# Performance work log

Measured on AMD Instinct MI355X. Metric: run time of the kernel, lower is better.

Reference implementation:

```python
import jax, jax.numpy as jnp
import numpy as np

BITS = 4
MAXQ = (1 << BITS) - 1  # 15
GROUPSIZE = 128
IN_F = 8192
OUT_F = 8192
PACK = 32 // BITS  # 8 values per int32


def setup_inputs() -> dict:
    key = jax.random.key(0)
    k_x, k_w, k_z, k_s, k_b = jax.random.split(key, 5)
    groups = IN_F // GROUPSIZE
    x = jax.random.normal(k_x, (4, 32, IN_F), dtype=jnp.float32)
    # bit-packed int32 weight / zeros (random bit patterns are valid quantized data)
    qweight = jax.random.randint(k_w, (IN_F // PACK, OUT_F), 0, 2**31 - 1, dtype=jnp.int32)
    qzeros = jax.random.randint(k_z, (groups, OUT_F // PACK), 0, 2**31 - 1, dtype=jnp.int32)
    scales = (jax.random.uniform(k_s, (groups, OUT_F), dtype=jnp.float32) * 0.01 + 1e-3)
    g_idx = (jnp.arange(IN_F, dtype=jnp.int32) // GROUPSIZE).astype(jnp.int32)
    bias = jax.random.normal(k_b, (OUT_F,), dtype=jnp.float32) * 0.01
    return {"x": x, "qweight": qweight, "qzeros": qzeros, "scales": scales,
            "g_idx": g_idx, "bias": bias}


def _dequant(qweight, qzeros, scales, g_idx):
    shifts = jnp.arange(0, 32, BITS, dtype=jnp.int32)  # [PACK]
    # unpack weights along the input dim: [in/PACK, PACK, out] -> [in, out]
    w = (qweight[:, None, :] >> shifts[None, :, None]) & MAXQ
    w = w.reshape(-1, qweight.shape[1])
    # unpack zeros along the output dim: [groups, out/PACK, PACK] -> [groups, out]
    # GPTQ stores (zero - 1), so add 1 back
    z = ((qzeros[:, :, None] >> shifts[None, None, :]) & MAXQ) + 1
    z = z.reshape(qzeros.shape[0], -1)
    # per-group dequant: W[i, o] = scales[g_idx[i], o] * (w[i, o] - z[g_idx[i], o])
    W = scales[g_idx] * (w.astype(scales.dtype) - z[g_idx].astype(scales.dtype))
    return W  # [in, out]


def reference(x, qweight, qzeros, scales, g_idx, bias):
    W = _dequant(qweight, qzeros, scales, g_idx)
    out = jnp.einsum('bsi,io->bso', x, W) + bias
    return out
```

## Files before the change

kernel.cpp:

```cpp
#include <hip/hip_runtime.h>
#include <hip/hip_bf16.h>
#include <stdint.h>


#define IN_F 8192
#define OUT_F 8192
#define MROWS 128
#define KSPLIT 8
#define KCHUNK 1024
#define BM 64

typedef short short8_t __attribute__((ext_vector_type(8)));
typedef float float4_t __attribute__((ext_vector_type(4)));
typedef float float16_t __attribute__((ext_vector_type(16)));

__global__ void reduce_out(const float* __restrict__ part, const float* __restrict__ bias,
                           float* __restrict__ out) {
  const int i = (blockIdx.x * 256 + threadIdx.x) * 4;
  const int o = i & (OUT_F - 1);
  float4_t s = *(const float4_t*)(bias + o);
#pragma unroll
  for (int sl = 0; sl < KSPLIT; ++sl)
    s += *(const float4_t*)(part + (size_t)sl * MROWS * OUT_F + i);
  *(float4_t*)(out + i) = s;
}

__global__ __launch_bounds__(1024, 4) void gptq_gemm(
    const float* __restrict__ x,
    const int* __restrict__ qweight,
    const int* __restrict__ qzeros,
    const float* __restrict__ scales,
    float* __restrict__ part)
{
  __shared__ unsigned short As[BM * KCHUNK];

  const int tid  = threadIdx.x;
  const int lane = tid & 63;
  const int l31  = lane & 31;
  const int half = lane >> 5;
  const int wv   = tid >> 6;

  const int bid = blockIdx.x;
  const int kb  = bid >> 5;
  const int mb  = (bid >> 4) & 1;
  const int nb  = bid & 15;

  const int kc0 = kb * KCHUNK;
  const int m0  = mb * BM;
  const int g0  = kc0 >> 7;
  const int kp_base = (kc0 >> 3) + half;

  const int col = nb * 512 + wv * 32 + l31;

  int   qw[3][8];
  float sc[3];
  int   zq[3];

  auto prefetch = [&](int gg, int buf) {
    const int kp = kp_base + gg * 16;
#pragma unroll
    for (int ks = 0; ks < 8; ++ks)
      qw[buf][ks] = qweight[(size_t)(kp + ks * 2) * OUT_F + col];
    const int gg_abs = g0 + gg;
    sc[buf] = scales[gg_abs * OUT_F + col];
    zq[buf] = qzeros[gg_abs * (OUT_F / 8) + (col >> 3)];
  };

  prefetch(0, 0);
  prefetch(1, 1);

  for (int rq = 0; rq < 4; ++rq) {
    const int rl = wv * 4 + rq;
    const float* grow = x + (size_t)(m0 + rl) * IN_F + kc0;
#pragma unroll
    for (int hf = 0; hf < 2; ++hf) {
      const int p = hf * 64 + lane;
      const int c = (p & 0x70) | ((p ^ (rl & 15)) & 15);
      float4_t a = *(const float4_t*)(grow + c * 8);
      float4_t b = *(const float4_t*)(grow + c * 8 + 4);
      union { short8_t v; __hip_bfloat162 h[4]; } u;
      u.h[0] = __float22bfloat162_rn(make_float2(a.x, a.y));
      u.h[1] = __float22bfloat162_rn(make_float2(a.z, a.w));
      u.h[2] = __float22bfloat162_rn(make_float2(b.x, b.y));
      u.h[3] = __float22bfloat162_rn(make_float2(b.z, b.w));
      *(short8_t*)(As + ((size_t)rl * 128 + p) * 8) = u.v;
    }
  }
  __syncthreads();

  float16_t acc[2];
#pragma unroll
  for (int mt = 0; mt < 2; ++mt)
#pragma unroll
    for (int r = 0; r < 16; ++r) acc[mt][r] = 0.f;

#pragma unroll
  for (int g = 0; g < 8; ++g) {
    const int cur = g % 3;

    if (g + 2 < 8) prefetch(g + 2, (g + 2) % 3);

    const int z = ((zq[cur] >> (4 * (col & 7))) & 15) + 1;
    const float zb = -sc[cur] * (float)z;
    const float s = sc[cur];

#pragma unroll
    for (int ks = 0; ks < 8; ++ks) {
      const int c = g * 16 + ks * 2 + half;
      const int p = (c & 0x70) | ((c ^ (l31 & 15)) & 15);

      short8_t af[2];
#pragma unroll
      for (int mt = 0; mt < 2; ++mt)
        af[mt] = *(const short8_t*)(As + ((size_t)(mt * 32 + l31) * 128 + p) * 8);

      union { short8_t v; unsigned u[4]; } bw;
      const unsigned q  = (unsigned)qw[cur][ks];
      const unsigned qe = q & 0x0F0F0F0Fu;
      const unsigned qo = (q >> 4) & 0x0F0F0F0Fu;
#pragma unroll
      for (int jj = 0; jj < 4; ++jj) {
        const float f0 = fmaf(s, (float)((qe >> (8 * jj)) & 0xffu), zb);
        const float f1 = fmaf(s, (float)((qo >> (8 * jj)) & 0xffu), zb);
        bw.u[jj] = __builtin_amdgcn_perm(__float_as_uint(f1), __float_as_uint(f0),
                                         0x07060302u);
      }

#pragma unroll
      for (int mt = 0; mt < 2; ++mt)
        acc[mt] = __builtin_amdgcn_mfma_f32_32x32x16_bf16(af[mt], bw.v, acc[mt], 0, 0, 0);
    }
  }

  float* base = part + (size_t)kb * (MROWS * OUT_F);
#pragma unroll
  for (int mt = 0; mt < 2; ++mt)
#pragma unroll
    for (int r = 0; r < 16; ++r) {
      const int row = (r & 3) + 8 * (r >> 2) + 4 * half;
      base[(size_t)(m0 + mt * 32 + row) * OUT_F + col] = acc[mt][r];
    }
}

extern "C" void kernel_launch(void* const* d_in, const int* in_sizes, int n_in,
                              void* d_out, int out_size, void* d_ws, size_t ws_size,
                              hipStream_t stream) {
  const float* x        = (const float*)d_in[0];
  const int*   qweight  = (const int*)d_in[1];
  const int*   qzeros   = (const int*)d_in[2];
  const float* scales   = (const float*)d_in[3];
  const float* bias     = (const float*)d_in[5];
  float* out = (float*)d_out;

  float* part = (float*)d_ws;

  gptq_gemm<<<dim3(256), 1024, 0, stream>>>(x, qweight, qzeros, scales, part);
  reduce_out<<<dim3((MROWS * OUT_F) / (256 * 4)), 256, 0, stream>>>(part, bias, out);
}
```

Measured before the change: 115.8 us.

## Store split-K partials as bf16 and stagger group order across waves

Measured after the change: 114.4 us. No clear change (-1.2%).

```diff
diff --git a/kernel.cpp b/kernel.cpp
--- a/kernel.cpp
+++ b/kernel.cpp
@@ -14,14 +14,21 @@
 typedef float float4_t __attribute__((ext_vector_type(4)));
 typedef float float16_t __attribute__((ext_vector_type(16)));
 
-__global__ void reduce_out(const float* __restrict__ part, const float* __restrict__ bias,
+__global__ void reduce_out(const unsigned short* __restrict__ part,
+                           const float* __restrict__ bias,
                            float* __restrict__ out) {
   const int i = (blockIdx.x * 256 + threadIdx.x) * 4;
   const int o = i & (OUT_F - 1);
   float4_t s = *(const float4_t*)(bias + o);
 #pragma unroll
-  for (int sl = 0; sl < KSPLIT; ++sl)
-    s += *(const float4_t*)(part + (size_t)sl * MROWS * OUT_F + i);
+  for (int sl = 0; sl < KSPLIT; ++sl) {
+    union { ushort2 u2[2]; unsigned short us[4]; } p;
+    *(uint2*)&p = *(const uint2*)(part + (size_t)sl * MROWS * OUT_F + i);
+    s.x += __uint_as_float((unsigned)p.us[0] << 16);
+    s.y += __uint_as_float((unsigned)p.us[1] << 16);
+    s.z += __uint_as_float((unsigned)p.us[2] << 16);
+    s.w += __uint_as_float((unsigned)p.us[3] << 16);
+  }
   *(float4_t*)(out + i) = s;
 }
 
@@ -30,7 +37,7 @@
     const int* __restrict__ qweight,
     const int* __restrict__ qzeros,
     const float* __restrict__ scales,
-    float* __restrict__ part)
+    unsigned short* __restrict__ part)
 {
   __shared__ unsigned short As[BM * KCHUNK];
 
@@ -49,6 +56,7 @@
   const int m0  = mb * BM;
   const int g0  = kc0 >> 7;
   const int kp_base = (kc0 >> 3) + half;
+  const int goff = (wv & 3) * 2;
 
   const int col = nb * 512 + wv * 32 + l31;
 
@@ -56,12 +64,13 @@
   float sc[3];
   int   zq[3];
 
-  auto prefetch = [&](int gg, int buf) {
-    const int kp = kp_base + gg * 16;
+  auto prefetch = [&](int i, int buf) {
+    const int ge = (i + goff) & 7;
+    const int kp = kp_base + ge * 16;
 #pragma unroll
     for (int ks = 0; ks < 8; ++ks)
       qw[buf][ks] = qweight[(size_t)(kp + ks * 2) * OUT_F + col];
-    const int gg_abs = g0 + gg;
+    const int gg_abs = g0 + ge;
     sc[buf] = scales[gg_abs * OUT_F + col];
     zq[buf] = qzeros[gg_abs * (OUT_F / 8) + (col >> 3)];
   };
@@ -97,6 +106,7 @@
 #pragma unroll
   for (int g = 0; g < 8; ++g) {
     const int cur = g % 3;
+    const int ge  = (g + goff) & 7;
 
     if (g + 2 < 8) prefetch(g + 2, (g + 2) % 3);
 
@@ -106,7 +116,7 @@
 
 #pragma unroll
     for (int ks = 0; ks < 8; ++ks) {
-      const int c = g * 16 + ks * 2 + half;
+      const int c = ge * 16 + ks * 2 + half;
       const int p = (c & 0x70) | ((c ^ (l31 & 15)) & 15);
 
       short8_t af[2];
@@ -132,13 +142,14 @@
     }
   }
 
-  float* base = part + (size_t)kb * (MROWS * OUT_F);
+  unsigned short* base = part + (size_t)kb * (MROWS * OUT_F);
 #pragma unroll
   for (int mt = 0; mt < 2; ++mt)
 #pragma unroll
     for (int r = 0; r < 16; ++r) {
       const int row = (r & 3) + 8 * (r >> 2) + 4 * half;
-      base[(size_t)(m0 + mt * 32 + row) * OUT_F + col] = acc[mt][r];
+      __hip_bfloat16 h = __float2bfloat16(acc[mt][r]);
+      base[(size_t)(m0 + mt * 32 + row) * OUT_F + col] = *(unsigned short*)&h;
     }
 }
 
@@ -152,7 +163,7 @@
   const float* bias     = (const float*)d_in[5];
   float* out = (float*)d_out;
 
-  float* part = (float*)d_ws;
+  unsigned short* part = (unsigned short*)d_ws;
 
   gptq_gemm<<<dim3(256), 1024, 0, stream>>>(x, qweight, qzeros, scales, part);
   reduce_out<<<dim3((MROWS * OUT_F) / (256 * 4)), 256, 0, stream>>>(part, bias, out);
```
